# Kernel tuning notes

Hardware: AMD Instinct MI355X
Metric: run time of the kernel (lower is better)

Reference implementation:

```python
import jax, jax.numpy as jnp
import numpy as np

IDIM = 128   # idim == odim (fc1 input dim must match shift-slice width idim_q)
HDIM = 1024
CDIM = 256
IGNORE_OUT = 10000.0


def setup_inputs() -> dict:
    key = jax.random.key(0)
    ks = jax.random.split(key, 4)
    B, T = 4, 512
    x = jax.random.normal(ks[0], (B, T, IDIM), dtype=jnp.float32)
    y = jax.random.normal(ks[1], (B, T, IDIM), dtype=jnp.float32)
    # xavier-ish init for the two linears (bias zeroed, as in initialize())
    w1 = jax.random.normal(ks[2], (HDIM, IDIM), dtype=jnp.float32) / np.sqrt(IDIM).astype(np.float32)
    b1 = jnp.zeros((HDIM,), jnp.float32)
    w2 = jax.random.normal(ks[3], (IDIM, HDIM), dtype=jnp.float32) / np.sqrt(HDIM).astype(np.float32)
    b2 = jnpts = jnp.zeros((IDIM,), jnp.float32)
    return {"x": x, "y": y, "w1": w1, "b1": b1, "w2": w2, "b2": b2}


def _shift_stack(key_seq, idim):
    """Vectorized _pad_for_shift: (B,T,idim) -> (B,T,2*idim-1,idim) shifted slices."""
    pad = idim - 1
    kp = jnp.pad(key_seq, ((0, 0), (0, 0), (pad, pad)))  # (B,T,3*idim-2)
    idx = jnp.arange(2 * idim - 1)[:, None] + jnp.arange(idim)[None, :]  # (S, idim)
    return kp[..., idx]  # (B,T,S,idim)


def _forward(x, y, w1, b1, w2, b2):
    idim = IDIM
    n_iter = HDIM // CDIM
    seq_mask = (y == IGNORE_OUT)                      # (B,T,odim)
    denom = jnp.sum(~seq_mask).astype(x.dtype)
    y_res, x_res = y, x
    losses = []
    for i in range(n_iter):
        # --- argaug (scale=False): sliding cosine cross-correlation + argmax ---
        kpt = _shift_stack(x_res, idim)               # (B,T,S,idim), S=2*idim-1
        num = jnp.einsum('btd,btsd->bts', y_res, kpt)
        den = jnp.linalg.norm(y_res, axis=-1)[..., None] * jnp.linalg.norm(kpt, axis=-1)
        sim = jnp.where(den == 0, 0.0, num / jnp.where(den == 0, 1.0, den))  # NaN(0/0) -> 0
        idx = jnp.argmax(sim, axis=-1)                # (B,T), first max like torch.max
        x_aug = jnp.take_along_axis(kpt, idx[..., None, None], axis=2)[..., 0, :]  # (B,T,idim)
        # --- attention (detached) ---
        attn = jax.lax.stop_gradient(jax.nn.softmax(x_aug * y_res, axis=-1))
        x_attn = x_aug * attn
        # --- _reverse_pad_for_shift: un-shift x_attn by 2*idim-2 - idx ---
        pad = idim - 1
        xap = jnp.pad(x_attn, ((0, 0), (0, 0), (pad, pad)))
        ridx = (2 * idim - 2 - idx)[..., None] + jnp.arange(idim)  # (B,T,idim)
        x_ele = jnp.take_along_axis(xap, ridx, axis=-1)
        # --- channel-masked two-layer MLP ---
        h = x_attn @ w1.T + b1                        # (B,T,hdim)
        m = jnp.zeros((HDIM,), x.dtype).at[i * CDIM:(i + 1) * CDIM].set(1.0)
        y_ele = (h * m) @ w2.T + b2                   # (B,T,odim)
        # --- masked MSE (sum of masked squared errors / #unmasked) ---
        sq = jnp.where(seq_mask, 0.0, (y_ele - y_res) ** 2)
        losses.append(jnp.sum(sq) / denom)
        y_res = y_res - y_ele
        x_res = x_res - x_ele
    return jnp.mean(jnp.stack(losses))


def reference(x, y, w1, b1, w2, b2):
    return _forward(x, y, w1, b1, w2, b2)
```

## Files before the change

kernel.cpp:

```cpp
#include <hip/hip_runtime.h>
#include <math.h>

#define NROWS 2048
#define NBLK  2048
#define NITER 4
#define IGNORE_OUT 10000.0f

__device__ __forceinline__ float readlanef(float v, int lane){
  return __int_as_float(__builtin_amdgcn_readlane(__float_as_int(v), lane));
}
__device__ __forceinline__ float gather128(float v0, float v1, int idx){
  float g0 = __shfl(v0, idx & 63, 64);
  float g1 = __shfl(v1, idx & 63, 64);
  float r  = (idx & 64) ? g1 : g0;
  return ((unsigned)idx < 128u) ? r : 0.f;
}
__device__ __forceinline__ float bflySum(float v){
  #pragma unroll
  for (int o = 32; o; o >>= 1) v += __shfl_xor(v, o, 64);
  return v;
}

__global__ __launch_bounds__(128)
void prepK(const float* __restrict__ w1, const float* __restrict__ b1,
           const float* __restrict__ w2, const float* __restrict__ b2,
           float* __restrict__ M4, float* __restrict__ biasT, int* __restrict__ ticket){
  const int blk = blockIdx.x;
  const int u = threadIdx.x;
  if (blk < 512){
    int i = blk >> 7, o = blk & 127;
    const float* w1p = w1 + (i * 256) * 128 + u;
    const float* w2p = w2 + o * 1024 + i * 256;
    float a = 0.f;
    #pragma unroll 16
    for (int c = 0; c < 256; ++c) a = fmaf(w1p[c * 128], w2p[c], a);
    M4[i * 16384 + (u >> 2) * 512 + o * 4 + (u & 3)] = a;
  } else if (blk < 516){
    int i = blk - 512;
    const float* w2p = w2 + u * 1024 + i * 256;
    const float* b1p = b1 + i * 256;
    float a = b2[u];
    #pragma unroll 8
    for (int c = 0; c < 256; ++c) a = fmaf(b1p[c], w2p[c], a);
    biasT[i * 128 + u] = a;
  } else {
    if (u == 0) *ticket = 0;
  }
}

__global__ __launch_bounds__(128, 4)
void mainK(const float* __restrict__ x, const float* __restrict__ y,
           const float* __restrict__ M4, const float* __restrict__ biasT,
           unsigned long long* __restrict__ partials, int* __restrict__ ticket,
           float* __restrict__ out){
  __shared__ float yd[384];
  __shared__ float yel[128];
  __shared__ float sVal[2];
  __shared__ int   sIdx[2];
  __shared__ float sL[2], sC[2];
  __shared__ int   sOld;

  const int u = threadIdx.x;
  const int l = u & 63;
  const int w = u >> 6;
  const long base = (long)blockIdx.x * 128;

  float xlo = x[base + l], xhi = x[base + 64 + l];
  float ylo = y[base + l], yhi = y[base + 64 + l];
  const float yOwn0 = w ? yhi : ylo;
  const bool mOwn = (yOwn0 == IGNORE_OUT);
  float cnt = mOwn ? 0.f : 1.f;
  float lossAcc = 0.f;

  yd[128 + u] = yOwn0; yd[256 + u] = yOwn0;
  __syncthreads();

  for (int i = 0; i < NITER; ++i){
    float own2 = w ? xhi * xhi : xlo * xlo;
    float oth2 = w ? xlo * xlo : xhi * xhi;
    float v = own2;
    #pragma unroll
    for (int o2 = 1; o2 < 64; o2 <<= 1){
      float tv = __shfl_up(v, o2, 64);
      if (l >= o2) v += tv;
    }
    float osum   = bflySum(oth2);
    float total  = readlanef(v, 63) + osum;
    float pref_t = w ? (v + osum) : v;

    float nY = sqrtf(bflySum(ylo * ylo + yhi * yhi));

    const float* wp = yd + (255 - u);
    float nt = 0.f, n1 = 0.f;
    if (w == 0){
      #pragma unroll 8
      for (int j = 0; j < 64; ++j){
        nt = fmaf(wp[j], readlanef(xlo, j), nt);
        n1 = (j == l) ? nt : n1;
      }
      #pragma unroll 8
      for (int j = 0; j < 64; ++j)
        nt = fmaf(wp[64 + j], readlanef(xhi, j), nt);
    } else {
      #pragma unroll 8
      for (int j = 0; j < 64; ++j)
        nt = fmaf(wp[j], readlanef(xlo, j), nt);
      n1 = nt;
      #pragma unroll 8
      for (int j = 0; j < 64; ++j){
        nt = fmaf(wp[64 + j], readlanef(xhi, j), nt);
        n1 = (j == l) ? nt : n1;
      }
    }

    {
      float num2 = nt - n1;
      float d1 = nY * sqrtf(pref_t);
      float d2 = nY * sqrtf(fmaxf(total - pref_t, 0.f));
      float s1 = (d1 == 0.f) ? 0.f : n1 / d1;
      float s2 = (d2 == 0.f) ? 0.f : num2 / d2;
      if (u == 127) s2 = -INFINITY;
      float bv = s1; int bi = u;
      if (s2 > bv){ bv = s2; bi = u + 128; }
      #pragma unroll
      for (int o2 = 1; o2 < 64; o2 <<= 1){
        float ov = __shfl_xor(bv, o2, 64);
        int   oi = __shfl_xor(bi, o2, 64);
        if (ov > bv || (ov == bv && oi < bi)){ bv = ov; bi = oi; }
      }
      if (l == 0){ sVal[w] = bv; sIdx[w] = bi; }
    }
    __syncthreads();
    int sstar;
    {
      float v0 = sVal[0], v1 = sVal[1];
      int   i0 = sIdx[0], i1 = sIdx[1];
      sstar = (v1 > v0 || (v1 == v0 && i1 < i0)) ? i1 : i0;
    }

    int j0 = sstar + l - 127;
    float xa = gather128(xlo, xhi, j0);
    float xb = gather128(xlo, xhi, j0 + 64);
    float ea = expf(xa * ylo), eb = expf(xb * yhi);
    float se = bflySum(ea + eb);
    float wlo = xa * (ea / se), whi = xb * (eb / se);

    int k0 = l + 127 - sstar;
    xlo -= gather128(wlo, whi, k0);
    xhi -= gather128(wlo, whi, k0 + 64);

    float ye;
    {
      const float4* Mp = (const float4*)(M4 + (size_t)i * 16384);
      float av = 0.f;
      #pragma unroll 4
      for (int dd = 0; dd < 16; ++dd){
        float4 m = Mp[dd * 128 + u];
        av = fmaf(m.x, readlanef(wlo, 4 * dd + 0), av);
        av = fmaf(m.y, readlanef(wlo, 4 * dd + 1), av);
        av = fmaf(m.z, readlanef(wlo, 4 * dd + 2), av);
        av = fmaf(m.w, readlanef(wlo, 4 * dd + 3), av);
      }
      #pragma unroll 4
      for (int dd = 16; dd < 32; ++dd){
        float4 m = Mp[dd * 128 + u];
        int b = 4 * dd - 64;
        av = fmaf(m.x, readlanef(whi, b + 0), av);
        av = fmaf(m.y, readlanef(whi, b + 1), av);
        av = fmaf(m.z, readlanef(whi, b + 2), av);
        av = fmaf(m.w, readlanef(whi, b + 3), av);
      }
      ye = av + biasT[i * 128 + u];
    }

    {
      float yOwn = w ? yhi : ylo;
      float df = ye - yOwn;
      if (!mOwn) lossAcc = fmaf(df, df, lossAcc);
      float yNew = yOwn - ye;
      yel[u] = ye;
      yd[128 + u] = yNew; yd[256 + u] = yNew;
    }
    __syncthreads();
    ylo = ylo - yel[l];
    yhi = yhi - yel[64 + l];
  }

  lossAcc = bflySum(lossAcc);
  cnt     = bflySum(cnt);
  if (l == 0){ sL[w] = lossAcc; sC[w] = cnt; }
  __syncthreads();
  if (u == 0){
    union { float2 f; unsigned long long v; } pk;
    pk.f.x = sL[0] + sL[1];
    pk.f.y = sC[0] + sC[1];
    __hip_atomic_store(&partials[blockIdx.x], pk.v, __ATOMIC_RELEASE, __HIP_MEMORY_SCOPE_AGENT);
    sOld = __hip_atomic_fetch_add(ticket, 1, __ATOMIC_ACQ_REL, __HIP_MEMORY_SCOPE_AGENT);
  }
  __syncthreads();
  if (sOld == NBLK - 1){
    float ls = 0.f, cs = 0.f;
    for (int g = u; g < NBLK; g += 128){
      union { float2 f; unsigned long long v; } pk;
      pk.v = __hip_atomic_load(&partials[g], __ATOMIC_ACQUIRE, __HIP_MEMORY_SCOPE_AGENT);
      ls += pk.f.x; cs += pk.f.y;
    }
    ls = bflySum(ls); cs = bflySum(cs);
    if (l == 0){ sL[w] = ls; sC[w] = cs; }
    __syncthreads();
    if (u == 0) out[0] = (sL[0] + sL[1]) / ((float)NITER * (sC[0] + sC[1]));
  }
}

extern "C" void kernel_launch(void* const* d_in, const int* in_sizes, int n_in,
                              void* d_out, int out_size, void* d_ws, size_t ws_size,
                              hipStream_t stream){
  const float* x  = (const float*)d_in[0];
  const float* y  = (const float*)d_in[1];
  const float* w1 = (const float*)d_in[2];
  const float* b1 = (const float*)d_in[3];
  const float* w2 = (const float*)d_in[4];
  const float* b2 = (const float*)d_in[5];
  float* out = (float*)d_out;

  int*   ticket = (int*)d_ws;
  float* M4     = (float*)((char*)d_ws + 256);
  float* biasT  = (float*)((char*)d_ws + 256 + 4 * 128 * 128 * sizeof(float));
  unsigned long long* partials =
      (unsigned long long*)((char*)d_ws + 256 + 4 * 128 * 128 * sizeof(float) + 4 * 128 * sizeof(float));

  prepK<<<517, 128, 0, stream>>>(w1, b1, w2, b2, M4, biasT, ticket);
  mainK<<<NBLK, 128, 0, stream>>>(x, y, M4, biasT, partials, ticket, out);
}
```

Measured before the change: 159.8 us.

## Use 4 shifted LDS copies of y for aligned float4 reads, fast intrinsics

The doubled y buffer in shared memory is replaced by four copies, each shifted by one element, so every thread can read its sliding window with aligned float4 LDS loads instead of scalar loads. The correlation loops are fully unrolled over these vector reads. Cosine normalisation now uses rsq intrinsics instead of sqrt and divide, and the softmax uses exp2 and rcp intrinsics instead of expf and division. In exchange each iteration does four times as many LDS writes, and the approximate intrinsics may change rounding, which could flip argmax ties.

After: 204.5 us. 1.28x slower.

```diff
diff --git a/kernel.cpp b/kernel.cpp
--- a/kernel.cpp
+++ b/kernel.cpp
@@ -5,6 +5,7 @@
 #define NBLK  2048
 #define NITER 4
 #define IGNORE_OUT 10000.0f
+#define LOG2E 1.44269504088896340736f
 
 __device__ __forceinline__ float readlanef(float v, int lane){
   return __int_as_float(__builtin_amdgcn_readlane(__float_as_int(v), lane));
@@ -53,7 +54,7 @@
            const float* __restrict__ M4, const float* __restrict__ biasT,
            unsigned long long* __restrict__ partials, int* __restrict__ ticket,
            float* __restrict__ out){
-  __shared__ float yd[384];
+  __shared__ alignas(16) float ydq[4][392];
   __shared__ float yel[128];
   __shared__ float sVal[2];
   __shared__ int   sIdx[2];
@@ -72,8 +73,15 @@
   float cnt = mOwn ? 0.f : 1.f;
   float lossAcc = 0.f;
 
-  yd[128 + u] = yOwn0; yd[256 + u] = yOwn0;
+  #pragma unroll
+  for (int k = 0; k < 4; ++k){
+    int m = u - k + 128;
+    ydq[k][m] = yOwn0; ydq[k][m + 128] = yOwn0;
+  }
   __syncthreads();
+
+  const int m0 = 255 - u;
+  const float4* wp4 = ((const float4*)&ydq[m0 & 3][0]) + (m0 >> 2);
 
   for (int i = 0; i < NITER; ++i){
     float own2 = w ? xhi * xhi : xlo * xlo;
@@ -88,37 +96,52 @@
     float total  = readlanef(v, 63) + osum;
     float pref_t = w ? (v + osum) : v;
 
-    float nY = sqrtf(bflySum(ylo * ylo + yhi * yhi));
-
-    const float* wp = yd + (255 - u);
+    float ny2 = bflySum(ylo * ylo + yhi * yhi);
+
     float nt = 0.f, n1 = 0.f;
     if (w == 0){
-      #pragma unroll 8
-      for (int j = 0; j < 64; ++j){
-        nt = fmaf(wp[j], readlanef(xlo, j), nt);
-        n1 = (j == l) ? nt : n1;
-      }
-      #pragma unroll 8
-      for (int j = 0; j < 64; ++j)
-        nt = fmaf(wp[64 + j], readlanef(xhi, j), nt);
+      #pragma unroll
+      for (int q = 0; q < 16; ++q){
+        float4 m4 = wp4[q]; int jb = 4 * q;
+        nt = fmaf(m4.x, readlanef(xlo, jb + 0), nt); n1 = (jb + 0 == l) ? nt : n1;
+        nt = fmaf(m4.y, readlanef(xlo, jb + 1), nt); n1 = (jb + 1 == l) ? nt : n1;
+        nt = fmaf(m4.z, readlanef(xlo, jb + 2), nt); n1 = (jb + 2 == l) ? nt : n1;
+        nt = fmaf(m4.w, readlanef(xlo, jb + 3), nt); n1 = (jb + 3 == l) ? nt : n1;
+      }
+      #pragma unroll
+      for (int q = 16; q < 32; ++q){
+        float4 m4 = wp4[q]; int jb = 4 * q - 64;
+        nt = fmaf(m4.x, readlanef(xhi, jb + 0), nt);
+        nt = fmaf(m4.y, readlanef(xhi, jb + 1), nt);
+        nt = fmaf(m4.z, readlanef(xhi, jb + 2), nt);
+        nt = fmaf(m4.w, readlanef(xhi, jb + 3), nt);
+      }
     } else {
-      #pragma unroll 8
-      for (int j = 0; j < 64; ++j)
-        nt = fmaf(wp[j], readlanef(xlo, j), nt);
+      #pragma unroll
+      for (int q = 0; q < 16; ++q){
+        float4 m4 = wp4[q]; int jb = 4 * q;
+        nt = fmaf(m4.x, readlanef(xlo, jb + 0), nt);
+        nt = fmaf(m4.y, readlanef(xlo, jb + 1), nt);
+        nt = fmaf(m4.z, readlanef(xlo, jb + 2), nt);
+        nt = fmaf(m4.w, readlanef(xlo, jb + 3), nt);
+      }
       n1 = nt;
-      #pragma unroll 8
-      for (int j = 0; j < 64; ++j){
-        nt = fmaf(wp[64 + j], readlanef(xhi, j), nt);
-        n1 = (j == l) ? nt : n1;
-      }
-    }
-
-    {
-      float num2 = nt - n1;
-      float d1 = nY * sqrtf(pref_t);
-      float d2 = nY * sqrtf(fmaxf(total - pref_t, 0.f));
-      float s1 = (d1 == 0.f) ? 0.f : n1 / d1;
-      float s2 = (d2 == 0.f) ? 0.f : num2 / d2;
+      #pragma unroll
+      for (int q = 16; q < 32; ++q){
+        float4 m4 = wp4[q]; int jb = 4 * q - 64;
+        nt = fmaf(m4.x, readlanef(xhi, jb + 0), nt); n1 = (jb + 0 == l) ? nt : n1;
+        nt = fmaf(m4.y, readlanef(xhi, jb + 1), nt); n1 = (jb + 1 == l) ? nt : n1;
+        nt = fmaf(m4.z, readlanef(xhi, jb + 2), nt); n1 = (jb + 2 == l) ? nt : n1;
+        nt = fmaf(m4.w, readlanef(xhi, jb + 3), nt); n1 = (jb + 3 == l) ? nt : n1;
+      }
+    }
+
+    {
+      bool yz = (ny2 == 0.f);
+      float rNY = __builtin_amdgcn_rsqf(ny2);
+      float nx2b = fmaxf(total - pref_t, 0.f);
+      float s1 = (yz || pref_t == 0.f) ? 0.f : n1 * __builtin_amdgcn_rsqf(pref_t) * rNY;
+      float s2 = (yz || nx2b  == 0.f) ? 0.f : (nt - n1) * __builtin_amdgcn_rsqf(nx2b) * rNY;
       if (u == 127) s2 = -INFINITY;
       float bv = s1; int bi = u;
       if (s2 > bv){ bv = s2; bi = u + 128; }
@@ -141,9 +164,10 @@
     int j0 = sstar + l - 127;
     float xa = gather128(xlo, xhi, j0);
     float xb = gather128(xlo, xhi, j0 + 64);
-    float ea = expf(xa * ylo), eb = expf(xb * yhi);
-    float se = bflySum(ea + eb);
-    float wlo = xa * (ea / se), whi = xb * (eb / se);
+    float ea = __builtin_amdgcn_exp2f(xa * ylo * LOG2E);
+    float eb = __builtin_amdgcn_exp2f(xb * yhi * LOG2E);
+    float rse = __builtin_amdgcn_rcpf(bflySum(ea + eb));
+    float wlo = xa * (ea * rse), whi = xb * (eb * rse);
 
     int k0 = l + 127 - sstar;
     xlo -= gather128(wlo, whi, k0);
@@ -179,7 +203,11 @@
       if (!mOwn) lossAcc = fmaf(df, df, lossAcc);
       float yNew = yOwn - ye;
       yel[u] = ye;
-      yd[128 + u] = yNew; yd[256 + u] = yNew;
+      #pragma unroll
+      for (int k = 0; k < 4; ++k){
+        int m = u - k + 128;
+        ydq[k][m] = yNew; ydq[k][m + 128] = yNew;
+      }
     }
     __syncthreads();
     ylo = ylo - yel[l];
```
